# Kernel tuning notes

Hardware: AMD Instinct MI355X
Metric: run time of the kernel (lower is better)

Reference implementation:

```python
import jax, jax.numpy as jnp
import numpy as np

N = 100000   # nodes
E = 1600000  # edges
D = 128      # input_dim
H = 128      # hidden_dim
G = 64       # graphs in batch
L = 3        # num GCN layers
BN_EPS = 1e-5


def setup_inputs() -> dict:
    key = jax.random.key(0)
    ks = jax.random.split(key, 16)
    s = 1.0 / np.sqrt(H)
    inp = {
        "x": jax.random.normal(ks[0], (N, D), jnp.float32),
        "edge_index": jax.random.randint(ks[1], (2, E), 0, N, dtype=jnp.int64),
        "batch": jnp.sort(jax.random.randint(ks[2], (N,), 0, G, dtype=jnp.int64)),
        # stacked GCNConv params (input_dim == hidden_dim so layer 0 stacks too)
        "conv_w": jax.random.normal(ks[3], (L, H, H), jnp.float32) * s,
        "conv_b": jax.random.normal(ks[4], (L, H), jnp.float32) * 0.01,
        # BatchNorm1d running stats + affine (eval mode)
        "bn_gamma": jnp.ones((L, H), jnp.float32),
        "bn_beta": jnp.zeros((L, H), jnp.float32),
        "bn_mean": jax.random.normal(ks[5], (L, H), jnp.float32) * 0.1,
        "bn_var": jax.random.uniform(ks[6], (L, H), jnp.float32, 0.5, 1.5),
        # node head MLP
        "node_w1": jax.random.normal(ks[7], (H // 2, H), jnp.float32) * s,
        "node_b1": jnp.zeros((H // 2,), jnp.float32),
        "node_w2": jax.random.normal(ks[8], (2, H // 2), jnp.float32) * (1.0 / np.sqrt(H // 2)),
        "node_b2": jnp.zeros((2,), jnp.float32),
        # graph head MLP
        "graph_w1": jax.random.normal(ks[9], (H // 2, H), jnp.float32) * s,
        "graph_b1": jnp.zeros((H // 2,), jnp.float32),
        "graph_w2": jax.random.normal(ks[10], (2, H // 2), jnp.float32) * (1.0 / np.sqrt(H // 2)),
        "graph_b2": jnp.zeros((2,), jnp.float32),
    }
    return inp


def _gcn_layer(h, src, dst, deg_inv_sqrt, w, b):
    # PyG GCNConv: h' = W h, then symmetric-normalized scatter-add over
    # edges (self-loops already appended to src/dst).
    h = h @ w.T                                   # [N, H]
    norm = deg_inv_sqrt[src] * deg_inv_sqrt[dst]  # [E+N]
    msg = h[src] * norm[:, None]                  # [E+N, H] gather
    out = jax.ops.segment_sum(msg, dst, num_segments=N)  # scatter-add
    return out + b


def _forward(x, edge_index, batch, conv_w, conv_b, bn_gamma, bn_beta,
             bn_mean, bn_var, node_w1, node_b1, node_w2, node_b2,
             graph_w1, graph_b1, graph_w2, graph_b2):
    loops = jnp.arange(N, dtype=edge_index.dtype)
    src = jnp.concatenate([edge_index[0], loops])
    dst = jnp.concatenate([edge_index[1], loops])
    deg = jax.ops.segment_sum(jnp.ones_like(src, dtype=x.dtype), dst,
                              num_segments=N)
    deg_inv_sqrt = jnp.where(deg > 0, jax.lax.rsqrt(deg), 0.0)

    h = x
    for i in range(L):  # conv -> BN(eval) -> ReLU (dropout inactive in eval)
        h = _gcn_layer(h, src, dst, deg_inv_sqrt, conv_w[i], conv_b[i])
        h = (h - bn_mean[i]) * jax.lax.rsqrt(bn_var[i] + BN_EPS) * bn_gamma[i] + bn_beta[i]
        h = jax.nn.relu(h)

    node_pred = jax.nn.relu(h @ node_w1.T + node_b1) @ node_w2.T + node_b2

    counts = jax.ops.segment_sum(jnp.ones((N,), h.dtype), batch,
                                 num_segments=G)
    graph_emb = jax.ops.segment_sum(h, batch, num_segments=G) / \
        jnp.maximum(counts, 1.0)[:, None]
    graph_pred = jax.nn.relu(graph_emb @ graph_w1.T + graph_b1) @ graph_w2.T + graph_b2
    return node_pred, graph_pred


def reference(x, edge_index, batch, conv_w, conv_b, bn_gamma, bn_beta,
              bn_mean, bn_var, node_w1, node_b1, node_w2, node_b2,
              graph_w1, graph_b1, graph_w2, graph_b2):
    return _forward(x, edge_index, batch, conv_w, conv_b, bn_gamma, bn_beta,
                    bn_mean, bn_var, node_w1, node_b1, node_w2, node_b2,
                    graph_w1, graph_b1, graph_w2, graph_b2)
```

## Files before the change

kernel.cpp:

```cpp
#include <hip/hip_runtime.h>
#include <hip/hip_bf16.h>

#define NN 100000
#define EE 1600000
#define HH 128
#define GG 64
#define LL 3
#define BN_EPS 1e-5f
#define NT 391
#define CHW 392
#define CAP 6144

typedef __hip_bfloat16 bf16;
typedef __attribute__((ext_vector_type(8))) short short8;
typedef __attribute__((ext_vector_type(4))) float floatx4;

__device__ __forceinline__ float lo16(unsigned v) { return __uint_as_float(v << 16); }
__device__ __forceinline__ float hi16(unsigned v) { return __uint_as_float(v & 0xffff0000u); }
__device__ __forceinline__ unsigned short f2b(float v) {
    bf16 h = __float2bfloat16(v);
    return *(unsigned short*)&h;
}
__device__ __forceinline__ unsigned pack2(float a, float b) {
    return (unsigned)f2b(a) | ((unsigned)f2b(b) << 16);
}
__device__ __forceinline__ int geti(const int* __restrict__ p, int i, int f) {
    return f ? p[2 * i] : p[i];
}

__global__ __launch_bounds__(1024) void k_part(const int* __restrict__ ei,
        unsigned* __restrict__ chunk, unsigned short* __restrict__ lbu,
        int* __restrict__ flag,
        const float* __restrict__ conv_w, const float* __restrict__ nw1,
        unsigned short* __restrict__ cwB, unsigned short* __restrict__ n1B,
        float* __restrict__ bnA, float* __restrict__ bnB,
        const float* __restrict__ conv_b, const float* __restrict__ g,
        const float* __restrict__ be, const float* __restrict__ mn,
        const float* __restrict__ vr, float* __restrict__ gsum,
        float* __restrict__ gcnt, unsigned* __restrict__ tbz) {
    __shared__ int lcnt[NT];
    __shared__ int sd[512];
    __shared__ unsigned short lbs[CHW];
    __shared__ unsigned sorted[4096];
    int t = threadIdx.x;
    int e0 = blockIdx.x * 4096;
    int probe = ei[2 * (e0 + (t & 63)) + 1];
    int f = __any(probe != 0) ? 0 : 1;
    if (blockIdx.x == 0 && t == 0) *flag = f;
    int gi = blockIdx.x * 1024 + t;
    if (gi < LL * HH * HH) cwB[gi] = f2b(conv_w[gi]);
    if (gi < 64 * HH) n1B[gi] = f2b(nw1[gi]);
    if (gi < LL * HH) {
        float A = g[gi] * rsqrtf(vr[gi] + BN_EPS);
        bnA[gi] = A;
        bnB[gi] = (conv_b[gi] - mn[gi]) * A + be[gi];
    }
    if (gi < GG * HH) gsum[gi] = 0.f;
    if (gi < GG) gcnt[gi] = 0.f;
    if (gi < 64) tbz[(size_t)NN * 64 + gi] = 0u;
    int nume = EE - e0 < 4096 ? EE - e0 : 4096;
    for (int i = t; i < NT; i += 1024) lcnt[i] = 0;
    __syncthreads();
    unsigned pk[4]; int ml[4], mt[4];
#pragma unroll
    for (int i = 0; i < 4; i++) {
        int li = i * 1024 + t;
        if (li < nume) {
            int e = e0 + li;
            int src = geti(ei, e, f), dst = geti(ei, EE + e, f);
            mt[i] = dst >> 8;
            pk[i] = ((unsigned)src << 8) | (unsigned)(dst & 255);
            ml[i] = atomicAdd(&lcnt[mt[i]], 1);
        }
    }
    __syncthreads();
    int own = 0;
    if (t < 512) {
        own = t < NT ? lcnt[t] : 0;
        sd[t] = own;
    }
    __syncthreads();
    for (int off = 1; off < 512; off <<= 1) {
        int y = 0;
        if (t < 512 && t >= off) y = sd[t - off];
        __syncthreads();
        if (t < 512) sd[t] += y;
        __syncthreads();
    }
    if (t < NT) lbs[t] = (unsigned short)(sd[t] - own);
    if (t == 0) lbs[NT] = (unsigned short)nume;
    __syncthreads();
#pragma unroll
    for (int i = 0; i < 4; i++) {
        int li = i * 1024 + t;
        if (li < nume) sorted[(int)lbs[mt[i]] + ml[i]] = pk[i];
    }
    if (t < CHW) lbu[blockIdx.x * CHW + t] = lbs[t];
    __syncthreads();
    for (int idx = t; idx < nume; idx += 1024)
        chunk[e0 + idx] = sorted[idx];
}

__global__ __launch_bounds__(1024) void k_csr(const unsigned* __restrict__ chunk,
        const unsigned short* __restrict__ lbu, unsigned* __restrict__ csr,
        int* __restrict__ offs, int* __restrict__ cnt, float* __restrict__ dinv) {
    __shared__ unsigned stage[CAP];
    __shared__ unsigned outb[CAP];
    __shared__ int sd[512];
    __shared__ int segso[512];
    __shared__ int segst[512];
    __shared__ int hist[256], exs[256], cur[256];
    __shared__ int s_nep;
    int T = blockIdx.x, t = threadIdx.x;
    int st = 0, rl = 0;
    if (t < NT) {
        int s0 = lbu[t * CHW + T];
        int s1 = lbu[t * CHW + T + 1];
        st = t * 4096 + s0;
        rl = s1 - s0;
    }
    if (t < 512) sd[t] = rl;
    __syncthreads();
    for (int off = 1; off < 512; off <<= 1) {
        int y = 0;
        if (t < 512 && t >= off) y = sd[t - off];
        __syncthreads();
        if (t < 512) sd[t] += y;
        __syncthreads();
    }
    int ne = sd[511];
    if (ne > CAP) ne = CAP;
    if (t < 512) {
        segso[t] = sd[t] - rl;
        segst[t] = st;
    }
    if (t < 256) hist[t] = 0;
    __syncthreads();
    for (int i = t; i < ne; i += 1024) {
        int lo = 0;
#pragma unroll
        for (int b = 256; b; b >>= 1) {
            int nlo = lo + b;
            if (nlo < 512 && segso[nlo] <= i) lo = nlo;
        }
        stage[i] = chunk[segst[lo] + (i - segso[lo])];
    }
    __syncthreads();
    for (int i = t; i < ne; i += 1024)
        atomicAdd(&hist[stage[i] & 255u], 1);
    __syncthreads();
    int c = 0, pc = 0;
    if (t < 256) {
        c = hist[t];
        pc = (c + 7) & ~7;
        exs[t] = pc;
    }
    __syncthreads();
    for (int off = 1; off < 256; off <<= 1) {
        int a = 0;
        if (t < 256 && t >= off) a = exs[t - off];
        __syncthreads();
        if (t < 256) exs[t] += a;
        __syncthreads();
    }
    if (t < 256) {
        int stn = exs[t] - pc;
        cur[t] = stn;
        int node = T * 256 + t;
        if (node < NN) {
            offs[node] = T * CAP + stn;
            cnt[node] = c;
            dinv[node] = rsqrtf(1.0f + (float)c);
        }
        for (int i = stn + c; i < stn + pc && i < CAP; i++)
            outb[i] = NN;
        if (t == 255) s_nep = exs[255] < CAP ? exs[255] : CAP;
    }
    __syncthreads();
    for (int i = t; i < ne; i += 1024) {
        unsigned p = stage[i];
        int q = atomicAdd(&cur[p & 255u], 1);
        if (q < CAP) outb[q] = p >> 8;
    }
    __syncthreads();
    int nep = s_nep;
    for (int i = t; i < nep; i += 1024)
        csr[(size_t)T * CAP + i] = outb[i];
}

template<typename AT, int NC, bool FUSE>
__global__ __launch_bounds__(256) void k_gemm(const AT* __restrict__ in,
        const unsigned short* __restrict__ Wb, const float* __restrict__ bias,
        unsigned short* __restrict__ outh, int do_relu,
        const float* __restrict__ scale,
        const float* __restrict__ w2, const float* __restrict__ b2v,
        float* __restrict__ out2f) {
    __shared__ char sB[NC * 272];
    int wave = threadIdx.x >> 6, lane = threadIdx.x & 63;
    int ln = lane & 15, q = lane >> 4;
    {
        const short8* wsrc = (const short8*)Wb;
        for (int i = threadIdx.x; i < NC * 16; i += 256) {
            short8 v = wsrc[i];
            *(short8*)(sB + (i >> 4) * 272 + (i & 15) * 16) = v;
        }
    }
    int r0 = blockIdx.x * 64 + wave * 16;
    int row = r0 + ln;
    int rr = row < NN ? row : NN - 1;
    short8 a[4];
    if constexpr (sizeof(AT) == 2) {
        const short8* ap = (const short8*)(in + (size_t)rr * HH);
#pragma unroll
        for (int kt = 0; kt < 4; kt++) a[kt] = ap[kt * 4 + q];
    } else {
        const float4* ap = (const float4*)(in + (size_t)rr * HH);
#pragma unroll
        for (int kt = 0; kt < 4; kt++) {
            float4 f0 = ap[(kt * 4 + q) * 2];
            float4 f1 = ap[(kt * 4 + q) * 2 + 1];
            a[kt][0] = (short)f2b(f0.x); a[kt][1] = (short)f2b(f0.y);
            a[kt][2] = (short)f2b(f0.z); a[kt][3] = (short)f2b(f0.w);
            a[kt][4] = (short)f2b(f1.x); a[kt][5] = (short)f2b(f1.y);
            a[kt][6] = (short)f2b(f1.z); a[kt][7] = (short)f2b(f1.w);
        }
    }
    float scl[4];
    if constexpr (!FUSE) {
#pragma unroll
        for (int reg = 0; reg < 4; reg++) {
            int orow = r0 + q * 4 + reg;
            scl[reg] = scale ? scale[orow < NN ? orow : NN - 1] : 1.f;
        }
    }
    __syncthreads();
    float p0[4], p1[4];
    if constexpr (FUSE) {
#pragma unroll
        for (int r = 0; r < 4; r++) { p0[r] = 0.f; p1[r] = 0.f; }
    }
#pragma unroll
    for (int ct = 0; ct < NC / 16; ct++) {
        int c = ct * 16 + ln;
        floatx4 acc = {0.f, 0.f, 0.f, 0.f};
#pragma unroll
        for (int kt = 0; kt < 4; kt++) {
            short8 b = *(const short8*)(sB + (size_t)c * 272 + kt * 64 + q * 16);
            acc = __builtin_amdgcn_mfma_f32_16x16x32_bf16(a[kt], b, acc, 0, 0, 0);
        }
        float bv = bias ? bias[c] : 0.f;
        if constexpr (FUSE) {
            float wa = w2[c], wb = w2[64 + c];
#pragma unroll
            for (int reg = 0; reg < 4; reg++) {
                float v = fmaxf(acc[reg] + bv, 0.f);
                p0[reg] = fmaf(v, wa, p0[reg]);
                p1[reg] = fmaf(v, wb, p1[reg]);
            }
        } else {
#pragma unroll
            for (int reg = 0; reg < 4; reg++) {
                int orow = r0 + q * 4 + reg;
                if (orow < NN) {
                    float v = acc[reg] + bv;
                    if (do_relu) v = fmaxf(v, 0.f);
                    outh[(size_t)orow * NC + c] = f2b(v * scl[reg]);
                }
            }
        }
    }
    if constexpr (FUSE) {
#pragma unroll
        for (int off = 1; off < 16; off <<= 1) {
#pragma unroll
            for (int r = 0; r < 4; r++) {
                p0[r] += __shfl_xor(p0[r], off);
                p1[r] += __shfl_xor(p1[r], off);
            }
        }
        if (ln == 0) {
            float ba = b2v[0], bb = b2v[1];
#pragma unroll
            for (int reg = 0; reg < 4; reg++) {
                int orow = r0 + q * 4 + reg;
                if (orow < NN)
                    ((float2*)out2f)[orow] = make_float2(p0[reg] + ba, p1[reg] + bb);
            }
        }
    }
}

__global__ __launch_bounds__(256) void k_aggr(const unsigned* __restrict__ tbs,
        const unsigned* __restrict__ csr, const int* __restrict__ offs,
        const int* __restrict__ cnt, const float* __restrict__ dinv,
        const float* __restrict__ bnA, const float* __restrict__ bnB,
        unsigned* __restrict__ hout) {
    int wave = threadIdx.x >> 6, lane = threadIdx.x & 63;
    int n0 = blockIdx.x * 8 + wave * 2;
    int n1 = n0 + 1;
    int base0 = __builtin_amdgcn_readfirstlane(offs[n0]);
    int base1 = __builtin_amdgcn_readfirstlane(offs[n1]);
    int ne0   = __builtin_amdgcn_readfirstlane(cnt[n0]);
    int ne1   = __builtin_amdgcn_readfirstlane(cnt[n1]);
    float dd0 = __uint_as_float(__builtin_amdgcn_readfirstlane(
                    (int)__float_as_uint(dinv[n0])));
    float dd1 = __uint_as_float(__builtin_amdgcn_readfirstlane(
                    (int)__float_as_uint(dinv[n1])));
    unsigned sv0 = tbs[(size_t)n0 * 64 + lane];
    unsigned sv1 = tbs[(size_t)n1 * 64 + lane];
    float ax0 = lo16(sv0), ay0 = hi16(sv0);
    float ax1 = lo16(sv1), ay1 = hi16(sv1);
    const unsigned* __restrict__ e0 = csr + base0;
    const unsigned* __restrict__ e1 = csr + base1;
    int nr0 = (ne0 + 7) & ~7, nr1 = (ne1 + 7) & ~7;
    int nr = nr0 > nr1 ? nr0 : nr1;
    for (int k0 = 0; k0 < nr; k0 += 8) {
        unsigned vv0[8], vv1[8];
        bool a0 = k0 < nr0, a1 = k0 < nr1;
        if (a0) {
#pragma unroll
            for (int j = 0; j < 8; j++) {
                int s = (int)e0[k0 + j];
                vv0[j] = tbs[(size_t)s * 64 + lane];
            }
        }
        if (a1) {
#pragma unroll
            for (int j = 0; j < 8; j++) {
                int s = (int)e1[k0 + j];
                vv1[j] = tbs[(size_t)s * 64 + lane];
            }
        }
        if (a0) {
#pragma unroll
            for (int j = 0; j < 8; j++) {
                ax0 += lo16(vv0[j]);
                ay0 += hi16(vv0[j]);
            }
        }
        if (a1) {
#pragma unroll
            for (int j = 0; j < 8; j++) {
                ax1 += lo16(vv1[j]);
                ay1 += hi16(vv1[j]);
            }
        }
    }
    float2 A = ((const float2*)bnA)[lane];
    float2 B = ((const float2*)bnB)[lane];
    float r0 = fmaxf(fmaf(ax0 * dd0, A.x, B.x), 0.f);
    float r1 = fmaxf(fmaf(ay0 * dd0, A.y, B.y), 0.f);
    float r2 = fmaxf(fmaf(ax1 * dd1, A.x, B.x), 0.f);
    float r3 = fmaxf(fmaf(ay1 * dd1, A.y, B.y), 0.f);
    __builtin_nontemporal_store(pack2(r0, r1), &hout[(size_t)n0 * 64 + lane]);
    __builtin_nontemporal_store(pack2(r2, r3), &hout[(size_t)n1 * 64 + lane]);
}

#define PN 32
__global__ __launch_bounds__(64) void k_pool(const unsigned* __restrict__ hb,
        const int* __restrict__ batch, float* __restrict__ gsum,
        float* __restrict__ gcnt, const int* __restrict__ flag) {
    int lane = threadIdx.x;
    int f = *flag;
    int s0 = blockIdx.x * PN;
    int cur = geti(batch, s0, f);
    float a0 = 0.f, a1 = 0.f, cn = 0.f;
    auto step = [&](int g, unsigned v) {
        if (g != cur) {
            atomicAdd(&gsum[cur * HH + 2 * lane], a0);
            atomicAdd(&gsum[cur * HH + 2 * lane + 1], a1);
            if (lane == 0) atomicAdd(&gcnt[cur], cn);
            a0 = a1 = cn = 0.f; cur = g;
        }
        a0 += lo16(v); a1 += hi16(v); cn += 1.f;
    };
    for (int n = s0; n < s0 + PN; n += 8) {
        int gg[8]; unsigned vv[8];
#pragma unroll
        for (int j = 0; j < 8; j++) {
            gg[j] = geti(batch, n + j, f);
            vv[j] = hb[(size_t)(n + j) * 64 + lane];
        }
#pragma unroll
        for (int j = 0; j < 8; j++) step(gg[j], vv[j]);
    }
    atomicAdd(&gsum[cur * HH + 2 * lane], a0);
    atomicAdd(&gsum[cur * HH + 2 * lane + 1], a1);
    if (lane == 0) atomicAdd(&gcnt[cur], cn);
}

__global__ __launch_bounds__(64) void k_ghead(const float* __restrict__ gsum,
        const float* __restrict__ gcnt, const float* __restrict__ w1,
        const float* __restrict__ b1, const float* __restrict__ w2,
        const float* __restrict__ b2v, float* __restrict__ out) {
    __shared__ float emb[HH];
    __shared__ float w1s[64 * 129];
    int g = blockIdx.x, lane = threadIdx.x;
    for (int gi = lane; gi < 64 * HH; gi += 64)
        w1s[(gi >> 7) * 129 + (gi & 127)] = w1[gi];
    float cn = gcnt[g];
    cn = cn > 1.f ? cn : 1.f;
    float inv = 1.f / cn;
    emb[lane] = gsum[g * HH + lane] * inv;
    emb[lane + 64] = gsum[g * HH + 64 + lane] * inv;
    __syncthreads();
    float acc = b1[lane];
    for (int k = 0; k < HH; k++) acc = fmaf(emb[k], w1s[lane * 129 + k], acc);
    float y = fmaxf(acc, 0.f);
    float v0 = y * w2[lane];
    float v1 = y * w2[64 + lane];
#pragma unroll
    for (int off = 32; off; off >>= 1) {
        v0 += __shfl_xor(v0, off);
        v1 += __shfl_xor(v1, off);
    }
    if (lane == 0) {
        out[(size_t)NN * 2 + g * 2]     = v0 + b2v[0];
        out[(size_t)NN * 2 + g * 2 + 1] = v1 + b2v[1];
    }
}

extern "C" void kernel_launch(void* const* d_in, const int* in_sizes, int n_in,
                              void* d_out, int out_size, void* d_ws, size_t ws_size,
                              hipStream_t stream) {
    const float* x      = (const float*)d_in[0];
    const int*   ei     = (const int*)d_in[1];
    const int*   batch  = (const int*)d_in[2];
    const float* conv_w = (const float*)d_in[3];
    const float* conv_b = (const float*)d_in[4];
    const float* bn_g   = (const float*)d_in[5];
    const float* bn_b   = (const float*)d_in[6];
    const float* bn_m   = (const float*)d_in[7];
    const float* bn_v   = (const float*)d_in[8];
    const float* nw1    = (const float*)d_in[9];
    const float* nb1    = (const float*)d_in[10];
    const float* nw2    = (const float*)d_in[11];
    const float* nb2    = (const float*)d_in[12];
    const float* gw1    = (const float*)d_in[13];
    const float* gb1    = (const float*)d_in[14];
    const float* gw2    = (const float*)d_in[15];
    const float* gb2    = (const float*)d_in[16];
    float* out = (float*)d_out;

    char* ws = (char*)d_ws;
    size_t off = 0;
    auto alloc = [&](size_t bytes) -> void* {
        void* p = ws + off;
        off += (bytes + 255) & ~(size_t)255;
        return p;
    };
    unsigned short* hb   = (unsigned short*)alloc((size_t)NN * HH * 2);
    unsigned short* tb   = (unsigned short*)alloc((size_t)(NN + 1) * HH * 2);
    unsigned* chunk  = (unsigned*)alloc((size_t)EE * 4);
    unsigned* csr    = (unsigned*)alloc((size_t)NT * CAP * 4);
    unsigned short* lbu = (unsigned short*)alloc((size_t)NT * CHW * 2);
    int*      offs   = (int*)     alloc((size_t)NN * 4);
    int*      cnt    = (int*)     alloc((size_t)NN * 4);
    float*    dinv   = (float*)   alloc((size_t)NN * 4);
    float*    bnA    = (float*)   alloc((size_t)LL * HH * 4);
    float*    bnB    = (float*)   alloc((size_t)LL * HH * 4);
    float*    gsum   = (float*)   alloc((size_t)GG * HH * 4);
    float*    gcnt   = (float*)   alloc((size_t)GG * 4);
    unsigned short* cwB = (unsigned short*)alloc((size_t)LL * HH * HH * 2);
    unsigned short* n1B = (unsigned short*)alloc((size_t)64 * HH * 2);
    int*      flag   = (int*)     alloc(256);

    k_part<<<NT, 1024, 0, stream>>>(ei, chunk, lbu, flag, conv_w, nw1, cwB, n1B,
            bnA, bnB, conv_b, bn_g, bn_b, bn_m, bn_v, gsum, gcnt, (unsigned*)tb);
    k_csr<<<NT, 1024, 0, stream>>>(chunk, lbu, csr, offs, cnt, dinv);

    k_gemm<float, HH, false><<<(NN + 63) / 64, 256, 0, stream>>>(
        x, cwB, nullptr, tb, 0, dinv, nullptr, nullptr, nullptr);
    k_aggr<<<NN / 8, 256, 0, stream>>>((const unsigned*)tb, csr, offs, cnt,
                                       dinv, bnA, bnB, (unsigned*)hb);
    for (int l = 1; l < LL; l++) {
        k_gemm<unsigned short, HH, false><<<(NN + 63) / 64, 256, 0, stream>>>(
            hb, cwB + (size_t)l * HH * HH, nullptr, tb, 0, dinv,
            nullptr, nullptr, nullptr);
        k_aggr<<<NN / 8, 256, 0, stream>>>((const unsigned*)tb, csr, offs,
                                           cnt, dinv, bnA + l * HH,
                                           bnB + l * HH, (unsigned*)hb);
    }

    k_gemm<unsigned short, 64, true><<<(NN + 63) / 64, 256, 0, stream>>>(
        hb, n1B, nb1, nullptr, 1, nullptr, nw2, nb2, out);

    k_pool<<<(NN + PN - 1) / PN, 64, 0, stream>>>((const unsigned*)hb, batch,
                                                  gsum, gcnt, flag);
    k_ghead<<<GG, 64, 0, stream>>>(gsum, gcnt, gw1, gb1, gw2, gb2, out);
}
```

Baseline: 417.8 us.

## Fuse graph mean-pooling into node-head GEMM and use wave-shuffle scans

Removes the separate k_pool kernel. Graph sums and counts are now accumulated inside the fused node-head GEMM from the A-operand registers it already holds, using segmented shuffle reductions plus atomics per graph segment. The LDS-based Hillis-Steele prefix scans in k_part and k_csr are replaced by wave-level __shfl_up scans with a small cross-wave combine, which cuts many __syncthreads. The aggregation output stores also switch from nontemporal to ordinary stores. This saves one launch and one full read of hb, at the cost of extra register pressure and shuffle work in the final GEMM, plus more atomics per 16-row group.

```diff
diff --git a/kernel.cpp b/kernel.cpp
--- a/kernel.cpp
+++ b/kernel.cpp
@@ -39,7 +39,7 @@
         const float* __restrict__ vr, float* __restrict__ gsum,
         float* __restrict__ gcnt, unsigned* __restrict__ tbz) {
     __shared__ int lcnt[NT];
-    __shared__ int sd[512];
+    __shared__ int wsum[8];
     __shared__ unsigned short lbs[CHW];
     __shared__ unsigned sorted[4096];
     int t = threadIdx.x;
@@ -74,20 +74,21 @@
         }
     }
     __syncthreads();
-    int own = 0;
-    if (t < 512) {
-        own = t < NT ? lcnt[t] : 0;
-        sd[t] = own;
-    }
-    __syncthreads();
-    for (int off = 1; off < 512; off <<= 1) {
-        int y = 0;
-        if (t < 512 && t >= off) y = sd[t - off];
-        __syncthreads();
-        if (t < 512) sd[t] += y;
-        __syncthreads();
-    }
-    if (t < NT) lbs[t] = (unsigned short)(sd[t] - own);
+    int own = 0, x = 0;
+    if (t < 512) { own = t < NT ? lcnt[t] : 0; x = own; }
+#pragma unroll
+    for (int off = 1; off < 64; off <<= 1) {
+        int y = __shfl_up(x, off);
+        if ((t & 63) >= off) x += y;
+    }
+    if (t < 512 && (t & 63) == 63) wsum[t >> 6] = x;
+    __syncthreads();
+    if (t < NT) {
+        int pre = 0, w = t >> 6;
+#pragma unroll
+        for (int i = 0; i < 7; i++) if (i < w) pre += wsum[i];
+        lbs[t] = (unsigned short)(pre + x - own);
+    }
     if (t == 0) lbs[NT] = (unsigned short)nume;
     __syncthreads();
 #pragma unroll
@@ -106,10 +107,11 @@
         int* __restrict__ offs, int* __restrict__ cnt, float* __restrict__ dinv) {
     __shared__ unsigned stage[CAP];
     __shared__ unsigned outb[CAP];
-    __shared__ int sd[512];
+    __shared__ int wsum[8];
+    __shared__ int w2[4];
     __shared__ int segso[512];
     __shared__ int segst[512];
-    __shared__ int hist[256], exs[256], cur[256];
+    __shared__ int hist[256], cur[256];
     __shared__ int s_nep;
     int T = blockIdx.x, t = threadIdx.x;
     int st = 0, rl = 0;
@@ -119,22 +121,26 @@
         st = t * 4096 + s0;
         rl = s1 - s0;
     }
-    if (t < 512) sd[t] = rl;
-    __syncthreads();
-    for (int off = 1; off < 512; off <<= 1) {
-        int y = 0;
-        if (t < 512 && t >= off) y = sd[t - off];
-        __syncthreads();
-        if (t < 512) sd[t] += y;
-        __syncthreads();
-    }
-    int ne = sd[511];
-    if (ne > CAP) ne = CAP;
+    int x = (t < 512) ? rl : 0;
+#pragma unroll
+    for (int off = 1; off < 64; off <<= 1) {
+        int y = __shfl_up(x, off);
+        if ((t & 63) >= off) x += y;
+    }
+    if (t < 512 && (t & 63) == 63) wsum[t >> 6] = x;
+    if (t < 256) hist[t] = 0;
+    __syncthreads();
+    int tot = 0;
+#pragma unroll
+    for (int i = 0; i < 8; i++) tot += wsum[i];
+    int ne = tot > CAP ? CAP : tot;
     if (t < 512) {
-        segso[t] = sd[t] - rl;
+        int pre = 0, w = t >> 6;
+#pragma unroll
+        for (int i = 0; i < 7; i++) if (i < w) pre += wsum[i];
+        segso[t] = pre + x - rl;
         segst[t] = st;
     }
-    if (t < 256) hist[t] = 0;
     __syncthreads();
     for (int i = t; i < ne; i += 1024) {
         int lo = 0;
@@ -149,22 +155,24 @@
     for (int i = t; i < ne; i += 1024)
         atomicAdd(&hist[stage[i] & 255u], 1);
     __syncthreads();
-    int c = 0, pc = 0;
+    int c = 0, pc = 0, x2 = 0;
     if (t < 256) {
         c = hist[t];
         pc = (c + 7) & ~7;
-        exs[t] = pc;
-    }
-    __syncthreads();
-    for (int off = 1; off < 256; off <<= 1) {
-        int a = 0;
-        if (t < 256 && t >= off) a = exs[t - off];
-        __syncthreads();
-        if (t < 256) exs[t] += a;
-        __syncthreads();
-    }
+        x2 = pc;
+    }
+#pragma unroll
+    for (int off = 1; off < 64; off <<= 1) {
+        int y = __shfl_up(x2, off);
+        if ((t & 63) >= off) x2 += y;
+    }
+    if (t < 256 && (t & 63) == 63) w2[t >> 6] = x2;
+    __syncthreads();
     if (t < 256) {
-        int stn = exs[t] - pc;
+        int pre = 0, w = t >> 6;
+#pragma unroll
+        for (int i = 0; i < 3; i++) if (i < w) pre += w2[i];
+        int stn = pre + x2 - pc;
         cur[t] = stn;
         int node = T * 256 + t;
         if (node < NN) {
@@ -174,7 +182,10 @@
         }
         for (int i = stn + c; i < stn + pc && i < CAP; i++)
             outb[i] = NN;
-        if (t == 255) s_nep = exs[255] < CAP ? exs[255] : CAP;
+    }
+    if (t == 0) {
+        int tt = w2[0] + w2[1] + w2[2] + w2[3];
+        s_nep = tt < CAP ? tt : CAP;
     }
     __syncthreads();
     for (int i = t; i < ne; i += 1024) {
@@ -194,7 +205,9 @@
         unsigned short* __restrict__ outh, int do_relu,
         const float* __restrict__ scale,
         const float* __restrict__ w2, const float* __restrict__ b2v,
-        float* __restrict__ out2f) {
+        float* __restrict__ out2f, float* __restrict__ gsum,
+        float* __restrict__ gcntp, const int* __restrict__ batchp,
+        const int* __restrict__ flagp) {
     __shared__ char sB[NC * 272];
     int wave = threadIdx.x >> 6, lane = threadIdx.x & 63;
     int ln = lane & 15, q = lane >> 4;
@@ -286,6 +299,41 @@
                 if (orow < NN)
                     ((float2*)out2f)[orow] = make_float2(p0[reg] + ba, p1[reg] + bb);
             }
+        }
+        int f = *flagp;
+        bool valid = row < NN;
+        int g = valid ? geti(batchp, row, f) : 0x7fffffff;
+        unsigned long long act = __ballot(valid);
+        int gbase = q * 16;
+        while (act) {
+            unsigned gmask = (unsigned)((act >> gbase) & 0xffffull);
+            int fl = gmask ? (__ffs((int)gmask) - 1) : 0;
+            int gcur = __shfl(g, gbase + fl);
+            bool m = (gmask != 0) && valid && (g == gcur);
+            float cw = m ? 1.f : 0.f;
+            float vs[32];
+#pragma unroll
+            for (int kt = 0; kt < 4; kt++)
+#pragma unroll
+                for (int j = 0; j < 8; j++)
+                    vs[kt * 8 + j] = m ? __uint_as_float(
+                        ((unsigned)(unsigned short)a[kt][j]) << 16) : 0.f;
+#pragma unroll
+            for (int off = 1; off < 16; off <<= 1) {
+                cw += __shfl_xor(cw, off);
+#pragma unroll
+                for (int v = 0; v < 32; v++) vs[v] += __shfl_xor(vs[v], off);
+            }
+            if (m && ln == fl) {
+#pragma unroll
+                for (int kt = 0; kt < 4; kt++)
+#pragma unroll
+                    for (int j = 0; j < 8; j++)
+                        atomicAdd(&gsum[gcur * HH + (kt * 4 + q) * 8 + j],
+                                  vs[kt * 8 + j]);
+                if (q == 0) atomicAdd(&gcntp[gcur], cw);
+            }
+            act &= ~__ballot(m);
         }
     }
 }
@@ -352,41 +400,8 @@
     float r1 = fmaxf(fmaf(ay0 * dd0, A.y, B.y), 0.f);
     float r2 = fmaxf(fmaf(ax1 * dd1, A.x, B.x), 0.f);
     float r3 = fmaxf(fmaf(ay1 * dd1, A.y, B.y), 0.f);
-    __builtin_nontemporal_store(pack2(r0, r1), &hout[(size_t)n0 * 64 + lane]);
-    __builtin_nontemporal_store(pack2(r2, r3), &hout[(size_t)n1 * 64 + lane]);
-}
-
-#define PN 32
-__global__ __launch_bounds__(64) void k_pool(const unsigned* __restrict__ hb,
-        const int* __restrict__ batch, float* __restrict__ gsum,
-        float* __restrict__ gcnt, const int* __restrict__ flag) {
-    int lane = threadIdx.x;
-    int f = *flag;
-    int s0 = blockIdx.x * PN;
-    int cur = geti(batch, s0, f);
-    float a0 = 0.f, a1 = 0.f, cn = 0.f;
-    auto step = [&](int g, unsigned v) {
-        if (g != cur) {
-            atomicAdd(&gsum[cur * HH + 2 * lane], a0);
-            atomicAdd(&gsum[cur * HH + 2 * lane + 1], a1);
-            if (lane == 0) atomicAdd(&gcnt[cur], cn);
-            a0 = a1 = cn = 0.f; cur = g;
-        }
-        a0 += lo16(v); a1 += hi16(v); cn += 1.f;
-    };
-    for (int n = s0; n < s0 + PN; n += 8) {
-        int gg[8]; unsigned vv[8];
-#pragma unroll
-        for (int j = 0; j < 8; j++) {
-            gg[j] = geti(batch, n + j, f);
-            vv[j] = hb[(size_t)(n + j) * 64 + lane];
-        }
-#pragma unroll
-        for (int j = 0; j < 8; j++) step(gg[j], vv[j]);
-    }
-    atomicAdd(&gsum[cur * HH + 2 * lane], a0);
-    atomicAdd(&gsum[cur * HH + 2 * lane + 1], a1);
-    if (lane == 0) atomicAdd(&gcnt[cur], cn);
+    hout[(size_t)n0 * 64 + lane] = pack2(r0, r1);
+    hout[(size_t)n1 * 64 + lane] = pack2(r2, r3);
 }
 
 __global__ __launch_bounds__(64) void k_ghead(const float* __restrict__ gsum,
@@ -470,22 +485,22 @@
     k_csr<<<NT, 1024, 0, stream>>>(chunk, lbu, csr, offs, cnt, dinv);
 
     k_gemm<float, HH, false><<<(NN + 63) / 64, 256, 0, stream>>>(
-        x, cwB, nullptr, tb, 0, dinv, nullptr, nullptr, nullptr);
+        x, cwB, nullptr, tb, 0, dinv, nullptr, nullptr, nullptr,
+        nullptr, nullptr, nullptr, nullptr);
     k_aggr<<<NN / 8, 256, 0, stream>>>((const unsigned*)tb, csr, offs, cnt,
                                        dinv, bnA, bnB, (unsigned*)hb);
     for (int l = 1; l < LL; l++) {
         k_gemm<unsigned short, HH, false><<<(NN + 63) / 64, 256, 0, stream>>>(
             hb, cwB + (size_t)l * HH * HH, nullptr, tb, 0, dinv,
-            nullptr, nullptr, nullptr);
+            nullptr, nullptr, nullptr, nullptr, nullptr, nullptr, nullptr);
         k_aggr<<<NN / 8, 256, 0, stream>>>((const unsigned*)tb, csr, offs,
                                            cnt, dinv, bnA + l * HH,
                                            bnB + l * HH, (unsigned*)hb);
     }
 
     k_gemm<unsigned short, 64, true><<<(NN + 63) / 64, 256, 0, stream>>>(
-        hb, n1B, nb1, nullptr, 1, nullptr, nw2, nb2, out);
-
-    k_pool<<<(NN + PN - 1) / PN, 64, 0, stream>>>((const unsigned*)hb, batch,
-                                                  gsum, gcnt, flag);
+        hb, n1B, nb1, nullptr, 1, nullptr, nw2, nb2, out,
+        gsum, gcnt, batch, flag);
+
     k_ghead<<<GG, 64, 0, stream>>>(gsum, gcnt, gw1, gb1, gw2, gb2, out);
 }
```

New measurement: 453.1 us. 8.5% more time.
